# Performance work log

Measured on AMD Instinct MI355X. Metric: run time of the kernel, lower is better.

The kernel has to match this reference:

```python
import jax, jax.numpy as jnp
import numpy as np

N, E, F_IN, D1, D2, D3, K, NL = 20000, 320000, 128, 256, 128, 64, 10, 4
EPS = 1e-5


def setup_inputs() -> dict:
    key = jax.random.key(0)
    ks = jax.random.split(key, 20)
    s = 0.05
    src = jax.random.randint(ks[1], (E,), 0, N)
    # avoid self-loops (PyG ChebConv removes them before building the Laplacian)
    dst = (src + 1 + jax.random.randint(ks[2], (E,), 0, N - 1)) % N
    return {
        "x": jax.random.normal(ks[0], (N, F_IN), jnp.float32),
        "edge_index": jnp.stack([src, dst]).astype(jnp.int64),
        "conv1_w": jax.random.normal(ks[3], (K, F_IN, D1), jnp.float32) * s,
        "convs_w": jax.random.normal(ks[4], (NL - 1, K, D1, D1), jnp.float32) * s,
        "convs_b": jax.random.normal(ks[5], (NL - 1, D1), jnp.float32) * s,
        "bn1_g": jnp.ones((D1,), jnp.float32),
        "bn1_b": jnp.zeros((D1,), jnp.float32),
        "fc1_w": jax.random.normal(ks[6], (D1, D2), jnp.float32) * s,
        "fc1_b": jax.random.normal(ks[7], (D2,), jnp.float32) * s,
        "bn2_g": jnp.ones((D2,), jnp.float32),
        "bn2_b": jnp.zeros((D2,), jnp.float32),
        "fc2_w": jax.random.normal(ks[8], (D2, D3), jnp.float32) * s,
        "fc2_b": jax.random.normal(ks[9], (D3,), jnp.float32) * s,
        "bn3_g": jnp.ones((D3,), jnp.float32),
        "bn3_b": jnp.zeros((D3,), jnp.float32),
        "fc3_w": jax.random.normal(ks[10], (D3, 1), jnp.float32) * s,
        "fc3_b": jax.random.normal(ks[11], (1,), jnp.float32) * s,
    }


def _lhat(h, src, dst, norm):
    # scaled Laplacian matvec: (L_sym - I) h  == scatter-add of norm * h[src] at dst
    return jax.ops.segment_sum(norm[:, None] * h[src], dst, num_segments=N)


def _cheb(h, W, b, src, dst, norm):
    # Chebyshev recurrence: T0=h, T1=L_hat h, Tk = 2 L_hat T(k-1) - T(k-2)
    Tx0 = h
    out = Tx0 @ W[0]
    Tx1 = _lhat(Tx0, src, dst, norm)
    out = out + Tx1 @ W[1]
    for k in range(2, W.shape[0]):
        Tx2 = 2.0 * _lhat(Tx1, src, dst, norm) - Tx0
        out = out + Tx2 @ W[k]
        Tx0, Tx1 = Tx1, Tx2
    return out if b is None else out + b


def _bn(h, g, b):
    # BatchNorm1d in training mode: batch stats, biased variance
    m = h.mean(axis=0)
    v = ((h - m) ** 2).mean(axis=0)
    return (h - m) * jax.lax.rsqrt(v + EPS) * g + b


def reference(x, edge_index, conv1_w, convs_w, convs_b, bn1_g, bn1_b,
              fc1_w, fc1_b, bn2_g, bn2_b, fc2_w, fc2_b, bn3_g, bn3_b,
              fc3_w, fc3_b):
    src, dst = edge_index[0], edge_index[1]
    deg = jax.ops.segment_sum(jnp.ones((E,), x.dtype), dst, num_segments=N)
    dinv = jnp.where(deg > 0, jax.lax.rsqrt(jnp.maximum(deg, 1.0)), 0.0)
    norm = -dinv[src] * dinv[dst]  # L_hat off-diagonal weights (lambda_max=2)

    h = jax.nn.relu(_cheb(x, conv1_w, None, src, dst, norm))
    for i in range(NL - 1):
        h = jax.nn.relu(_cheb(h, convs_w[i], convs_b[i], src, dst, norm))
        h = _bn(h, bn1_g, bn1_b)
    h = _bn(h @ fc1_w + fc1_b, bn2_g, bn2_b)
    h = jax.nn.relu(h)
    h = _bn(h @ fc2_w + fc2_b, bn3_g, bn3_b)
    return h @ fc3_w + fc3_b
```

## Files before the change

### kernel.cpp

```cpp
#include <hip/hip_runtime.h>
#include <hip/hip_bf16.h>
#include <stdint.h>


#define N_NODES 20000
#define N_EDGES 320000
#define FDIM_IN 128
#define DD1 256
#define DD2 128
#define DD3 64
#define K_CHEB 10
#define EPSBN 1e-5f
#define BN_B 512

typedef unsigned short u16;
typedef unsigned int u32;
typedef _Float16 half8 __attribute__((ext_vector_type(8)));
typedef __attribute__((ext_vector_type(4))) float floatx4;

__device__ __forceinline__ u16 f2h(float v) {
  _Float16 h = (_Float16)v;
  return *reinterpret_cast<u16*>(&h);
}

__device__ __forceinline__ void gld16(const void* g, void* l) {
  __builtin_amdgcn_global_load_lds((const __attribute__((address_space(1))) u32*)g,
                                   (__attribute__((address_space(3))) u32*)l, 16, 0, 0);
}

__global__ void detect_idx_kernel(const void* ei, int* flag) {
  int t = threadIdx.x;
  const int* p = (const int*)ei;
  int v = p[2 * t + 1];
  unsigned long long b = __ballot(v == 0);
  if (t == 0) *flag = (b == ~0ULL) ? 1 : 0;
}

__device__ __forceinline__ int load_edge(const void* ei, int mode64, long long pos) {
  return mode64 ? (int)((const long long*)ei)[pos] : ((const int*)ei)[pos];
}

__global__ void deg_kernel(const void* ei, const int* __restrict__ flag, int* __restrict__ ideg) {
  int e = blockIdx.x * blockDim.x + threadIdx.x;
  if (e < N_EDGES) {
    int d = load_edge(ei, *flag, (long long)N_EDGES + e);
    atomicAdd(&ideg[d], 1);
  }
}

__global__ void dinv_kernel(const int* __restrict__ ideg, float* __restrict__ dinv) {
  int n = blockIdx.x * blockDim.x + threadIdx.x;
  if (n < N_NODES) {
    int d = ideg[n];
    dinv[n] = d > 0 ? rsqrtf((float)d) : 0.f;
  }
}

__global__ __launch_bounds__(1024) void scan_kernel(const int* __restrict__ ideg, int* __restrict__ rowptr) {
  __shared__ int part[1024];
  int tid = threadIdx.x;
  const int CH = (N_NODES + 1023) / 1024;
  int base = tid * CH;
  int s = 0;
  for (int i = 0; i < CH; i++) { int idx = base + i; if (idx < N_NODES) s += ideg[idx]; }
  part[tid] = s;
  __syncthreads();
  for (int off = 1; off < 1024; off <<= 1) {
    int v = (tid >= off) ? part[tid - off] : 0;
    __syncthreads();
    part[tid] += v;
    __syncthreads();
  }
  int run = (tid == 0) ? 0 : part[tid - 1];
  for (int i = 0; i < CH; i++) { int idx = base + i; if (idx < N_NODES) { rowptr[idx] = run; run += ideg[idx]; } }
  if (tid == 1023) rowptr[N_NODES] = run;
}

__global__ void fill_csr_kernel(const void* ei, const int* __restrict__ flag,
                                const float* __restrict__ dinv, const int* __restrict__ rowptr,
                                int* __restrict__ cnt, int* __restrict__ col, float* __restrict__ wcsr) {
  int e = blockIdx.x * blockDim.x + threadIdx.x;
  if (e < N_EDGES) {
    int m = *flag;
    int s = load_edge(ei, m, e);
    int d = load_edge(ei, m, (long long)N_EDGES + e);
    int pos = rowptr[d] + atomicAdd(&cnt[d], 1);
    col[pos] = s;
    wcsr[pos] = -dinv[s] * dinv[d];
  }
}

__global__ __launch_bounds__(256) void wt_kernel(const float* __restrict__ W, u16* __restrict__ Wt,
                                                 int KF, int Nd) {
  __shared__ float sm[32][36];
  int kf0 = blockIdx.x * 32, n0 = blockIdx.y * 32;
  int r = threadIdx.x >> 3, c4 = (threadIdx.x & 7) * 4;
  float4 v = *(const float4*)(W + (size_t)(kf0 + r) * Nd + n0 + c4);
  sm[r][c4 + 0] = v.x; sm[r][c4 + 1] = v.y; sm[r][c4 + 2] = v.z; sm[r][c4 + 3] = v.w;
  __syncthreads();
  int on = threadIdx.x >> 3, okf4 = (threadIdx.x & 7) * 4;
  ushort4 u;
  u.x = f2h(sm[okf4 + 0][on]);
  u.y = f2h(sm[okf4 + 1][on]);
  u.z = f2h(sm[okf4 + 2][on]);
  u.w = f2h(sm[okf4 + 3][on]);
  *(ushort4*)(Wt + (size_t)(n0 + on) * KF + kf0 + okf4) = u;
}

template <int F>
__global__ void convert_cat_kernel(const float* __restrict__ in, u16* __restrict__ cat) {
  constexpr int F8 = F / 8;
  int i = blockIdx.x * blockDim.x + threadIdx.x;
  int n = i / F8, f8 = i % F8;
  const float4* p = (const float4*)(in + (size_t)n * F + f8 * 8);
  float4 a = p[0], b = p[1];
  half8 o;
  o[0] = (_Float16)a.x; o[1] = (_Float16)a.y; o[2] = (_Float16)a.z; o[3] = (_Float16)a.w;
  o[4] = (_Float16)b.x; o[5] = (_Float16)b.y; o[6] = (_Float16)b.z; o[7] = (_Float16)b.w;
  *(half8*)(cat + (size_t)n * (10 * F) + f8 * 8) = o;
}

template <int F, bool HAS_TX0>
__global__ void lhat5_kernel(u16* __restrict__ cat,
                             const int* __restrict__ rowptr, const int* __restrict__ col,
                             const float* __restrict__ w, float scale,
                             int inOff, int tx0Off, int outOff) {
  constexpr int R = 10 * F;
  constexpr int SLICES = F / 64;
  constexpr int NPG = N_NODES * SLICES / 8;
  int xcd = blockIdx.x & 7;
  int lb = blockIdx.x >> 3;
  int q = xcd % SLICES;
  int grp = xcd / SLICES;
  int node0 = grp * NPG;
  int node = node0 + lb * 32 + (threadIdx.x >> 3);
  if (node >= node0 + NPG || node >= N_NODES) return;
  int ln8 = q * 64 + (threadIdx.x & 7) * 8;
  int beg = rowptr[node], end = rowptr[node + 1];
  float acc[8] = {0.f, 0.f, 0.f, 0.f, 0.f, 0.f, 0.f, 0.f};
  int e = beg;
  for (; e + 7 < end; e += 8) {
    int c[8];
    float wv[8];
#pragma unroll
    for (int j = 0; j < 8; j++) { c[j] = col[e + j]; wv[j] = w[e + j]; }
    half8 v[8];
#pragma unroll
    for (int j = 0; j < 8; j++) v[j] = *(const half8*)(cat + (size_t)c[j] * R + inOff + ln8);
#pragma unroll
    for (int j = 0; j < 8; j++)
#pragma unroll
      for (int i = 0; i < 8; i++) acc[i] += wv[j] * (float)v[j][i];
  }
  if (e + 3 < end) {
    int c[4];
    float wv[4];
#pragma unroll
    for (int j = 0; j < 4; j++) { c[j] = col[e + j]; wv[j] = w[e + j]; }
    half8 v[4];
#pragma unroll
    for (int j = 0; j < 4; j++) v[j] = *(const half8*)(cat + (size_t)c[j] * R + inOff + ln8);
#pragma unroll
    for (int j = 0; j < 4; j++)
#pragma unroll
      for (int i = 0; i < 8; i++) acc[i] += wv[j] * (float)v[j][i];
    e += 4;
  }
  for (; e < end; e++) {
    int c0 = col[e];
    float w0 = w[e];
    half8 v0 = *(const half8*)(cat + (size_t)c0 * R + inOff + ln8);
#pragma unroll
    for (int i = 0; i < 8; i++) acc[i] += w0 * (float)v0[i];
  }
  float r[8];
#pragma unroll
  for (int i = 0; i < 8; i++) r[i] = scale * acc[i];
  if (HAS_TX0) {
    half8 t = *(const half8*)(cat + (size_t)node * R + tx0Off + ln8);
#pragma unroll
    for (int i = 0; i < 8; i++) r[i] -= (float)t[i];
  }
  half8 o;
#pragma unroll
  for (int i = 0; i < 8; i++) o[i] = (_Float16)r[i];
  *(half8*)(cat + (size_t)node * R + outOff + ln8) = o;
}

__global__ __launch_bounds__(256) void gemm_cat_kernel(
    const u16* __restrict__ A, int ldA, const u16* __restrict__ B, int ldB, int kBase,
    int Kc, float* __restrict__ C, int ldC, int Nc, const float* __restrict__ bias, int M,
    int NX, int NY, int accFlag, int reluFlag) {
  __shared__ __align__(16) u16 As[64 * 64];
  __shared__ __align__(16) u16 Bs[64 * 64];
  int pid = blockIdx.x;
  int g8 = 8 * NY;
  int a8 = pid / g8, rem = pid % g8;
  int by = rem >> 3;
  int bx = a8 * 8 + (rem & 7);
  if (bx >= NX) return;
  int tid = threadIdx.x;
  int lane = tid & 63, wave = tid >> 6;
  int wr = wave >> 1, wc = wave & 1;
  int l15 = lane & 15, l16 = lane >> 4;
  int m0 = bx * 64, n0 = by * 64;
  floatx4 acc[2][2];
#pragma unroll
  for (int m = 0; m < 2; m++)
#pragma unroll
    for (int n = 0; n < 2; n++) acc[m][n] = (floatx4){0.f, 0.f, 0.f, 0.f};

  int subrow = lane >> 3;
  int bcol = (lane & 7) * 16;

  for (int k0 = 0; k0 < Kc; k0 += 64) {
    __syncthreads();
#pragma unroll
    for (int i = 0; i < 4; i++) {
      int c = wave * 4 + i;
      if (c < 8) {
        int row = c * 8 + subrow;
        const char* src = (const char*)A + ((size_t)(m0 + row) * ldA + kBase + k0) * 2 +
                          (bcol ^ ((row & 7) << 4));
        gld16(src, (char*)As + c * 1024);
      } else {
        int row = (c - 8) * 8 + subrow;
        const char* src = (const char*)B + ((size_t)(n0 + row) * ldB + kBase + k0) * 2 +
                          (bcol ^ ((row & 7) << 4));
        gld16(src, (char*)Bs + (c - 8) * 1024);
      }
    }
    __syncthreads();
#pragma unroll
    for (int kk = 0; kk < 2; kk++) {
      int kb = kk * 64 + l16 * 16;
      half8 a[2];
#pragma unroll
      for (int m = 0; m < 2; m++) {
        int r = wr * 32 + m * 16 + l15;
        a[m] = *(half8*)((char*)As + r * 128 + (kb ^ ((r & 7) << 4)));
      }
#pragma unroll
      for (int n = 0; n < 2; n++) {
        int r = wc * 32 + n * 16 + l15;
        half8 b = *(half8*)((char*)Bs + r * 128 + (kb ^ ((r & 7) << 4)));
        acc[0][n] = __builtin_amdgcn_mfma_f32_16x16x32_f16(a[0], b, acc[0][n], 0, 0, 0);
        acc[1][n] = __builtin_amdgcn_mfma_f32_16x16x32_f16(a[1], b, acc[1][n], 0, 0, 0);
      }
    }
  }
#pragma unroll
  for (int m = 0; m < 2; m++)
#pragma unroll
    for (int n = 0; n < 2; n++)
#pragma unroll
      for (int j = 0; j < 4; j++) {
        int row = m0 + wr * 32 + m * 16 + l16 * 4 + j;
        int colI = n0 + wc * 32 + n * 16 + l15;
        if (row < M && colI < Nc) {
          size_t idx = (size_t)row * ldC + colI;
          float v = acc[m][n][j];
          if (accFlag) v += C[idx];
          if (bias) v += bias[colI];
          if (reluFlag) v = fmaxf(v, 0.f);
          C[idx] = v;
        }
      }
}

template <int D>
__global__ __launch_bounds__(256) void bn_part_kernel(const float* __restrict__ h,
                                                      float* __restrict__ part, int rows) {
  constexpr int TPR = D / 4;
  constexpr int RPI = 256 / TPR;
  __shared__ float4 ssum[256], ssq[256];
  int tid = threadIdx.x;
  int g = tid / TPR;
  int fr = tid % TPR;
  float4 s = {0.f, 0.f, 0.f, 0.f}, q = {0.f, 0.f, 0.f, 0.f};
  for (int r = blockIdx.x * RPI + g; r < rows; r += gridDim.x * RPI) {
    float4 v = *(const float4*)(h + (size_t)r * D + fr * 4);
    s.x += v.x; s.y += v.y; s.z += v.z; s.w += v.w;
    q.x += v.x * v.x; q.y += v.y * v.y; q.z += v.z * v.z; q.w += v.w * v.w;
  }
  ssum[tid] = s; ssq[tid] = q;
  __syncthreads();
  if (g == 0) {
#pragma unroll
    for (int gg = 1; gg < RPI; gg++) {
      float4 a = ssum[gg * TPR + fr], b = ssq[gg * TPR + fr];
      s.x += a.x; s.y += a.y; s.z += a.z; s.w += a.w;
      q.x += b.x; q.y += b.y; q.z += b.z; q.w += b.w;
    }
    *(float4*)(part + (size_t)blockIdx.x * (2 * D) + fr * 4) = s;
    *(float4*)(part + (size_t)blockIdx.x * (2 * D) + D + fr * 4) = q;
  }
}

__global__ void bn_reduce_kernel(const float* __restrict__ part, float* __restrict__ acc, int D) {
  int c = blockIdx.x;
  int tid = threadIdx.x;
  float v = 0.f;
  for (int b = tid; b < BN_B; b += 64) v += part[(size_t)b * (2 * D) + c];
#pragma unroll
  for (int off = 32; off > 0; off >>= 1) v += __shfl_down(v, off);
  if (tid == 0) {
    if (c < D) acc[c] = v;
    else acc[256 + (c - D)] = v;
  }
}

template <int D>
__global__ void bn_apply_kernel(float* __restrict__ h, const float* __restrict__ acc,
                                const float* __restrict__ gam, const float* __restrict__ bet,
                                int rows, int relu, float invRows,
                                u16* __restrict__ dst16, int ld16) {
  constexpr int F4 = D / 4;
  int i = blockIdx.x * blockDim.x + threadIdx.x;
  if (i >= rows * F4) return;
  int row = i / F4;
  int fi = (i % F4) * 4;
  float4 s4 = *(const float4*)(acc + fi);
  float4 q4 = *(const float4*)(acc + 256 + fi);
  float4 g4 = *(const float4*)(gam + fi);
  float4 b4 = *(const float4*)(bet + fi);
  float4 v = *(float4*)(h + (size_t)row * D + fi);
  float4 res;
  {
    float m = s4.x * invRows, var = q4.x * invRows - m * m;
    res.x = (v.x - m) * rsqrtf(var + EPSBN) * g4.x + b4.x;
    m = s4.y * invRows; var = q4.y * invRows - m * m;
    res.y = (v.y - m) * rsqrtf(var + EPSBN) * g4.y + b4.y;
    m = s4.z * invRows; var = q4.z * invRows - m * m;
    res.z = (v.z - m) * rsqrtf(var + EPSBN) * g4.z + b4.z;
    m = s4.w * invRows; var = q4.w * invRows - m * m;
    res.w = (v.w - m) * rsqrtf(var + EPSBN) * g4.w + b4.w;
  }
  if (relu) {
    res.x = fmaxf(res.x, 0.f); res.y = fmaxf(res.y, 0.f);
    res.z = fmaxf(res.z, 0.f); res.w = fmaxf(res.w, 0.f);
  }
  *(float4*)(h + (size_t)row * D + fi) = res;
  if (dst16) {
    ushort4 u;
    u.x = f2h(res.x); u.y = f2h(res.y); u.z = f2h(res.z); u.w = f2h(res.w);
    *(ushort4*)(dst16 + (size_t)row * ld16 + fi) = u;
  }
}

__global__ void fc3_kernel(const float* __restrict__ h, const float* __restrict__ w,
                           const float* __restrict__ b, float* __restrict__ out) {
  int node = blockIdx.x * 4 + (threadIdx.x >> 6);
  int lane = threadIdx.x & 63;
  if (node >= N_NODES) return;
  float v = h[(size_t)node * DD3 + lane] * w[lane];
#pragma unroll
  for (int off = 32; off > 0; off >>= 1) v += __shfl_down(v, off);
  if (lane == 0) out[node] = v + b[0];
}

extern "C" void kernel_launch(void* const* d_in, const int* in_sizes, int n_in,
                              void* d_out, int out_size, void* d_ws, size_t ws_size,
                              hipStream_t stream) {
  const float* x = (const float*)d_in[0];
  const void* ei = d_in[1];
  const float* conv1_w = (const float*)d_in[2];
  const float* convs_w = (const float*)d_in[3];
  const float* convs_b = (const float*)d_in[4];
  const float* bn1_g = (const float*)d_in[5];
  const float* bn1_b = (const float*)d_in[6];
  const float* fc1_w = (const float*)d_in[7];
  const float* fc1_b = (const float*)d_in[8];
  const float* bn2_g = (const float*)d_in[9];
  const float* bn2_b = (const float*)d_in[10];
  const float* fc2_w = (const float*)d_in[11];
  const float* fc2_b = (const float*)d_in[12];
  const float* bn3_g = (const float*)d_in[13];
  const float* bn3_b = (const float*)d_in[14];
  const float* fc3_w = (const float*)d_in[15];
  const float* fc3_b = (const float*)d_in[16];
  float* out = (float*)d_out;

  char* ws = (char*)d_ws;
  size_t off = 0;
  auto alloc = [&](size_t bytes) -> void* {
    off = (off + 255) & ~(size_t)255;
    void* p = ws + off;
    off += bytes;
    return p;
  };
  u16* Tcat = (u16*)alloc((size_t)(N_NODES + 64) * 10 * DD1 * 2);
  float* bufA = (float*)alloc((size_t)N_NODES * DD1 * 4);
  float* bufB = (float*)alloc((size_t)N_NODES * DD1 * 4);
  float* f1buf = (float*)alloc((size_t)N_NODES * DD2 * 4);
  float* f2buf = (float*)alloc((size_t)N_NODES * DD3 * 4);
  u16* h16 = (u16*)alloc((size_t)(N_NODES + 64) * DD1 * 2);
  u16* h16b = (u16*)alloc((size_t)(N_NODES + 64) * DD2 * 2);
  u16* Wt = (u16*)alloc((size_t)(1280 * 256 + 3 * 2560 * 256) * 2);
  u16* Wtf1 = (u16*)alloc((size_t)DD2 * DD1 * 2);
  u16* Wtf2 = (u16*)alloc((size_t)128 * DD2 * 2);
  float* bnpart = (float*)alloc((size_t)BN_B * 2 * DD1 * 4);
  int* ideg = (int*)alloc(N_NODES * 4);
  int* rowptr = (int*)alloc((N_NODES + 1) * 4);
  int* cnt = (int*)alloc(N_NODES * 4);
  int* col = (int*)alloc(N_EDGES * 4);
  float* wcsr = (float*)alloc(N_EDGES * 4);
  float* dinv = (float*)alloc(N_NODES * 4);
  float* bnacc = (float*)alloc(512 * 4);
  int* flag = (int*)alloc(4);
  if (off > ws_size) return;

  wt_kernel<<<dim3(1280 / 32, 8), 256, 0, stream>>>(conv1_w, Wt, 1280, 256);
  for (int l = 0; l < 3; l++)
    wt_kernel<<<dim3(2560 / 32, 8), 256, 0, stream>>>(convs_w + (size_t)l * 655360,
                                                      Wt + 327680 + (size_t)l * 655360, 2560, 256);
  wt_kernel<<<dim3(256 / 32, 128 / 32), 256, 0, stream>>>(fc1_w, Wtf1, 256, 128);
  wt_kernel<<<dim3(128 / 32, 64 / 32), 256, 0, stream>>>(fc2_w, Wtf2, 128, 64);

  hipMemsetAsync(ideg, 0, N_NODES * 4, stream);
  hipMemsetAsync(cnt, 0, N_NODES * 4, stream);
  detect_idx_kernel<<<1, 64, 0, stream>>>(ei, flag);
  deg_kernel<<<(N_EDGES + 255) / 256, 256, 0, stream>>>(ei, flag, ideg);
  dinv_kernel<<<(N_NODES + 255) / 256, 256, 0, stream>>>(ideg, dinv);
  scan_kernel<<<1, 1024, 0, stream>>>(ideg, rowptr);
  fill_csr_kernel<<<(N_EDGES + 255) / 256, 256, 0, stream>>>(ei, flag, dinv, rowptr, cnt, col, wcsr);

  auto lhat = [&](int F, float scale, int inS, int tx0S, int outS) {
    if (F == 128) {
      if (tx0S < 0)
        lhat5_kernel<128, false><<<8 * 157, 256, 0, stream>>>(Tcat, rowptr, col, wcsr, scale,
                                                              inS * 128, 0, outS * 128);
      else
        lhat5_kernel<128, true><<<8 * 157, 256, 0, stream>>>(Tcat, rowptr, col, wcsr, scale,
                                                             inS * 128, tx0S * 128, outS * 128);
    } else {
      if (tx0S < 0)
        lhat5_kernel<256, false><<<8 * 313, 256, 0, stream>>>(Tcat, rowptr, col, wcsr, scale,
                                                              inS * 256, 0, outS * 256);
      else
        lhat5_kernel<256, true><<<8 * 313, 256, 0, stream>>>(Tcat, rowptr, col, wcsr, scale,
                                                             inS * 256, tx0S * 256, outS * 256);
    }
  };
  auto mgemm = [&](const u16* A, int ldA, const u16* B, int ldB, int kBase, int Kc,
                   float* C, int ldC, int Nc, const float* bias, int accFlag, int relu) {
    int NX = (N_NODES + 63) / 64;
    int NXP = (NX + 7) & ~7;
    int NY = (Nc + 63) / 64;
    gemm_cat_kernel<<<dim3(NXP * NY), 256, 0, stream>>>(A, ldA, B, ldB, kBase, Kc, C, ldC, Nc,
                                                        bias, N_NODES, NX, NY, accFlag, relu);
  };
  auto cheb = [&](int F, const u16* WtL, const float* bias, float* hout, int relu) {
    lhat(F, 1.f, 0, -1, 1);
    for (int k = 2; k < K_CHEB; k++) lhat(F, 2.f, k - 1, k - 2, k);
    mgemm(Tcat, 10 * F, WtL, 10 * F, 0, 10 * F, hout, 256, 256, bias, 0, relu);
  };
  auto bn = [&](float* h, int D, const float* g, const float* b, int relu, u16* dst16, int ld16) {
    if (D == 256) {
      bn_part_kernel<256><<<BN_B, 256, 0, stream>>>(h, bnpart, N_NODES);
      bn_reduce_kernel<<<2 * 256, 64, 0, stream>>>(bnpart, bnacc, 256);
      bn_apply_kernel<256><<<(N_NODES * 64 + 255) / 256, 256, 0, stream>>>(
          h, bnacc, g, b, N_NODES, relu, 1.f / N_NODES, dst16, ld16);
    } else if (D == 128) {
      bn_part_kernel<128><<<BN_B, 256, 0, stream>>>(h, bnpart, N_NODES);
      bn_reduce_kernel<<<2 * 128, 64, 0, stream>>>(bnpart, bnacc, 128);
      bn_apply_kernel<128><<<(N_NODES * 32 + 255) / 256, 256, 0, stream>>>(
          h, bnacc, g, b, N_NODES, relu, 1.f / N_NODES, dst16, ld16);
    } else {
      bn_part_kernel<64><<<BN_B, 256, 0, stream>>>(h, bnpart, N_NODES);
      bn_reduce_kernel<<<2 * 64, 64, 0, stream>>>(bnpart, bnacc, 64);
      bn_apply_kernel<64><<<(N_NODES * 16 + 255) / 256, 256, 0, stream>>>(
          h, bnacc, g, b, N_NODES, relu, 1.f / N_NODES, dst16, ld16);
    }
  };

  convert_cat_kernel<128><<<1250, 256, 0, stream>>>(x, Tcat);
  cheb(FDIM_IN, Wt, nullptr, bufA, 1);

  convert_cat_kernel<256><<<2500, 256, 0, stream>>>(bufA, Tcat);
  cheb(DD1, Wt + 327680, convs_b, bufB, 1);
  bn(bufB, DD1, bn1_g, bn1_b, 0, Tcat, 10 * DD1);

  cheb(DD1, Wt + 327680 + 655360, convs_b + DD1, bufA, 1);
  bn(bufA, DD1, bn1_g, bn1_b, 0, Tcat, 10 * DD1);

  cheb(DD1, Wt + 327680 + 2 * 655360, convs_b + 2 * DD1, bufB, 1);
  bn(bufB, DD1, bn1_g, bn1_b, 0, h16, DD1);

  mgemm(h16, DD1, Wtf1, DD1, 0, DD1, f1buf, DD2, DD2, fc1_b, 0, 0);
  bn(f1buf, DD2, bn2_g, bn2_b, 1, h16b, DD2);

  mgemm(h16b, DD2, Wtf2, DD2, 0, DD2, f2buf, DD3, DD3, fc2_b, 0, 0);
  bn(f2buf, DD3, bn3_g, bn3_b, 0, nullptr, 0);

  fc3_kernel<<<(N_NODES + 3) / 4, 256, 0, stream>>>(f2buf, fc3_w, fc3_b, out);
}
```

Measured before the change: 1.099 ms.

## Split edge loop across two thread groups per node and fuse fp16 convert into GEMM

```diff
diff --git a/kernel.cpp b/kernel.cpp
--- a/kernel.cpp
+++ b/kernel.cpp
@@ -121,7 +121,7 @@
 }
 
 template <int F, bool HAS_TX0>
-__global__ void lhat5_kernel(u16* __restrict__ cat,
+__global__ void lhat6_kernel(u16* __restrict__ cat,
                              const int* __restrict__ rowptr, const int* __restrict__ col,
                              const float* __restrict__ w, float scale,
                              int inOff, int tx0Off, int outOff) {
@@ -133,64 +133,58 @@
   int q = xcd % SLICES;
   int grp = xcd / SLICES;
   int node0 = grp * NPG;
-  int node = node0 + lb * 32 + (threadIdx.x >> 3);
+  int node = node0 + lb * 16 + (threadIdx.x >> 4);
   if (node >= node0 + NPG || node >= N_NODES) return;
+  int g = (threadIdx.x >> 3) & 1;
   int ln8 = q * 64 + (threadIdx.x & 7) * 8;
   int beg = rowptr[node], end = rowptr[node + 1];
   float acc[8] = {0.f, 0.f, 0.f, 0.f, 0.f, 0.f, 0.f, 0.f};
-  int e = beg;
-  for (; e + 7 < end; e += 8) {
-    int c[8];
-    float wv[8];
-#pragma unroll
-    for (int j = 0; j < 8; j++) { c[j] = col[e + j]; wv[j] = w[e + j]; }
-    half8 v[8];
-#pragma unroll
-    for (int j = 0; j < 8; j++) v[j] = *(const half8*)(cat + (size_t)c[j] * R + inOff + ln8);
-#pragma unroll
-    for (int j = 0; j < 8; j++)
-#pragma unroll
-      for (int i = 0; i < 8; i++) acc[i] += wv[j] * (float)v[j][i];
-  }
-  if (e + 3 < end) {
-    int c[4];
-    float wv[4];
-#pragma unroll
-    for (int j = 0; j < 4; j++) { c[j] = col[e + j]; wv[j] = w[e + j]; }
-    half8 v[4];
-#pragma unroll
-    for (int j = 0; j < 4; j++) v[j] = *(const half8*)(cat + (size_t)c[j] * R + inOff + ln8);
-#pragma unroll
-    for (int j = 0; j < 4; j++)
-#pragma unroll
-      for (int i = 0; i < 8; i++) acc[i] += wv[j] * (float)v[j][i];
-    e += 4;
-  }
-  for (; e < end; e++) {
-    int c0 = col[e];
-    float w0 = w[e];
-    half8 v0 = *(const half8*)(cat + (size_t)c0 * R + inOff + ln8);
-#pragma unroll
-    for (int i = 0; i < 8; i++) acc[i] += w0 * (float)v0[i];
-  }
-  float r[8];
-#pragma unroll
-  for (int i = 0; i < 8; i++) r[i] = scale * acc[i];
-  if (HAS_TX0) {
-    half8 t = *(const half8*)(cat + (size_t)node * R + tx0Off + ln8);
-#pragma unroll
-    for (int i = 0; i < 8; i++) r[i] -= (float)t[i];
-  }
-  half8 o;
-#pragma unroll
-  for (int i = 0; i < 8; i++) o[i] = (_Float16)r[i];
-  *(half8*)(cat + (size_t)node * R + outOff + ln8) = o;
+  for (int e0 = beg + g * 8; e0 < end; e0 += 16) {
+    int n = end - e0;
+    if (n >= 8) {
+      int c[8];
+      float wv[8];
+#pragma unroll
+      for (int j = 0; j < 8; j++) { c[j] = col[e0 + j]; wv[j] = w[e0 + j]; }
+      half8 v[8];
+#pragma unroll
+      for (int j = 0; j < 8; j++) v[j] = *(const half8*)(cat + (size_t)c[j] * R + inOff + ln8);
+#pragma unroll
+      for (int j = 0; j < 8; j++)
+#pragma unroll
+        for (int i = 0; i < 8; i++) acc[i] += wv[j] * (float)v[j][i];
+    } else {
+      for (int j = 0; j < n; j++) {
+        int c0 = col[e0 + j];
+        float w0 = w[e0 + j];
+        half8 v0 = *(const half8*)(cat + (size_t)c0 * R + inOff + ln8);
+#pragma unroll
+        for (int i = 0; i < 8; i++) acc[i] += w0 * (float)v0[i];
+      }
+    }
+  }
+#pragma unroll
+  for (int i = 0; i < 8; i++) acc[i] += __shfl_xor(acc[i], 8);
+  if (g == 0) {
+    float r[8];
+#pragma unroll
+    for (int i = 0; i < 8; i++) r[i] = scale * acc[i];
+    if (HAS_TX0) {
+      half8 t = *(const half8*)(cat + (size_t)node * R + tx0Off + ln8);
+#pragma unroll
+      for (int i = 0; i < 8; i++) r[i] -= (float)t[i];
+    }
+    half8 o;
+#pragma unroll
+    for (int i = 0; i < 8; i++) o[i] = (_Float16)r[i];
+    *(half8*)(cat + (size_t)node * R + outOff + ln8) = o;
+  }
 }
 
 __global__ __launch_bounds__(256) void gemm_cat_kernel(
     const u16* __restrict__ A, int ldA, const u16* __restrict__ B, int ldB, int kBase,
     int Kc, float* __restrict__ C, int ldC, int Nc, const float* __restrict__ bias, int M,
-    int NX, int NY, int accFlag, int reluFlag) {
+    int NX, int NY, int accFlag, int reluFlag, u16* __restrict__ dst16, int ld16) {
   __shared__ __align__(16) u16 As[64 * 64];
   __shared__ __align__(16) u16 Bs[64 * 64];
   int pid = blockIdx.x;
@@ -264,6 +258,7 @@
           if (bias) v += bias[colI];
           if (reluFlag) v = fmaxf(v, 0.f);
           C[idx] = v;
+          if (dst16) dst16[(size_t)row * ld16 + colI] = f2h(v);
         }
       }
 }
@@ -428,32 +423,35 @@
   auto lhat = [&](int F, float scale, int inS, int tx0S, int outS) {
     if (F == 128) {
       if (tx0S < 0)
-        lhat5_kernel<128, false><<<8 * 157, 256, 0, stream>>>(Tcat, rowptr, col, wcsr, scale,
+        lhat6_kernel<128, false><<<8 * 313, 256, 0, stream>>>(Tcat, rowptr, col, wcsr, scale,
                                                               inS * 128, 0, outS * 128);
       else
-        lhat5_kernel<128, true><<<8 * 157, 256, 0, stream>>>(Tcat, rowptr, col, wcsr, scale,
+        lhat6_kernel<128, true><<<8 * 313, 256, 0, stream>>>(Tcat, rowptr, col, wcsr, scale,
                                                              inS * 128, tx0S * 128, outS * 128);
     } else {
       if (tx0S < 0)
-        lhat5_kernel<256, false><<<8 * 313, 256, 0, stream>>>(Tcat, rowptr, col, wcsr, scale,
+        lhat6_kernel<256, false><<<8 * 625, 256, 0, stream>>>(Tcat, rowptr, col, wcsr, scale,
                                                               inS * 256, 0, outS * 256);
       else
-        lhat5_kernel<256, true><<<8 * 313, 256, 0, stream>>>(Tcat, rowptr, col, wcsr, scale,
+        lhat6_kernel<256, true><<<8 * 625, 256, 0, stream>>>(Tcat, rowptr, col, wcsr, scale,
                                                              inS * 256, tx0S * 256, outS * 256);
     }
   };
   auto mgemm = [&](const u16* A, int ldA, const u16* B, int ldB, int kBase, int Kc,
-                   float* C, int ldC, int Nc, const float* bias, int accFlag, int relu) {
+                   float* C, int ldC, int Nc, const float* bias, int accFlag, int relu,
+                   u16* dst16, int ld16) {
     int NX = (N_NODES + 63) / 64;
     int NXP = (NX + 7) & ~7;
     int NY = (Nc + 63) / 64;
     gemm_cat_kernel<<<dim3(NXP * NY), 256, 0, stream>>>(A, ldA, B, ldB, kBase, Kc, C, ldC, Nc,
-                                                        bias, N_NODES, NX, NY, accFlag, relu);
+                                                        bias, N_NODES, NX, NY, accFlag, relu,
+                                                        dst16, ld16);
   };
-  auto cheb = [&](int F, const u16* WtL, const float* bias, float* hout, int relu) {
+  auto cheb = [&](int F, const u16* WtL, const float* bias, float* hout, int relu,
+                  u16* dst16, int ld16) {
     lhat(F, 1.f, 0, -1, 1);
     for (int k = 2; k < K_CHEB; k++) lhat(F, 2.f, k - 1, k - 2, k);
-    mgemm(Tcat, 10 * F, WtL, 10 * F, 0, 10 * F, hout, 256, 256, bias, 0, relu);
+    mgemm(Tcat, 10 * F, WtL, 10 * F, 0, 10 * F, hout, 256, 256, bias, 0, relu, dst16, ld16);
   };
   auto bn = [&](float* h, int D, const float* g, const float* b, int relu, u16* dst16, int ld16) {
     if (D == 256) {
@@ -475,22 +473,21 @@
   };
 
   convert_cat_kernel<128><<<1250, 256, 0, stream>>>(x, Tcat);
-  cheb(FDIM_IN, Wt, nullptr, bufA, 1);
-
-  convert_cat_kernel<256><<<2500, 256, 0, stream>>>(bufA, Tcat);
-  cheb(DD1, Wt + 327680, convs_b, bufB, 1);
+  cheb(FDIM_IN, Wt, nullptr, bufA, 1, Tcat, 10 * DD1);
+
+  cheb(DD1, Wt + 327680, convs_b, bufB, 1, nullptr, 0);
   bn(bufB, DD1, bn1_g, bn1_b, 0, Tcat, 10 * DD1);
 
-  cheb(DD1, Wt + 327680 + 655360, convs_b + DD1, bufA, 1);
+  cheb(DD1, Wt + 327680 + 655360, convs_b + DD1, bufA, 1, nullptr, 0);
   bn(bufA, DD1, bn1_g, bn1_b, 0, Tcat, 10 * DD1);
 
-  cheb(DD1, Wt + 327680 + 2 * 655360, convs_b + 2 * DD1, bufB, 1);
+  cheb(DD1, Wt + 327680 + 2 * 655360, convs_b + 2 * DD1, bufB, 1, nullptr, 0);
   bn(bufB, DD1, bn1_g, bn1_b, 0, h16, DD1);
 
-  mgemm(h16, DD1, Wtf1, DD1, 0, DD1, f1buf, DD2, DD2, fc1_b, 0, 0);
+  mgemm(h16, DD1, Wtf1, DD1, 0, DD1, f1buf, DD2, DD2, fc1_b, 0, 0, nullptr, 0);
   bn(f1buf, DD2, bn2_g, bn2_b, 1, h16b, DD2);
 
-  mgemm(h16b, DD2, Wtf2, DD2, 0, DD2, f2buf, DD3, DD3, fc2_b, 0, 0);
+  mgemm(h16b, DD2, Wtf2, DD2, 0, DD2, f2buf, DD3, DD3, fc2_b, 0, 0, nullptr, 0);
   bn(f2buf, DD3, bn3_g, bn3_b, 0, nullptr, 0);
 
   fc3_kernel<<<(N_NODES + 3) / 4, 256, 0, stream>>>(f2buf, fc3_w, fc3_b, out);
```

After: 1.754 ms. +59.6%, slower.
